# Optimization experiments

Measured on AMD Instinct MI355X. Metric: run time of the kernel, lower is better.

The kernel has to match this reference:

```python
import jax, jax.numpy as jnp
import numpy as np

T = 64        # n_estimators
DEPTH = 8
D = 2**DEPTH - 1   # internal nodes per tree (255)
K = 2**DEPTH       # leaves per tree (256)
M = 512       # n_features
C = 8         # class_num
B = 4096      # batch


def _build_path_masks():
    # Complete binary tree in heap order. For leaf l, walk from root;
    # going LEFT corresponds to b==+1 -> multiply (1 - x_node) -> Bpos,
    # going RIGHT corresponds to b==-1 -> multiply x_node -> Bneg.
    Bpos = np.zeros((K, D), dtype=np.float32)
    Bneg = np.zeros((K, D), dtype=np.float32)
    for l in range(K):
        node = 0
        for level in range(DEPTH):
            bit = (l >> (DEPTH - 1 - level)) & 1
            if bit == 0:
                Bpos[l, node] = 1.0
            else:
                Bneg[l, node] = 1.0
            node = 2 * node + 1 + bit
    return Bpos, Bneg


def setup_inputs() -> dict:
    rng = np.random.default_rng(0)
    key = jax.random.key(0)
    x = jax.random.normal(key, (B, M), dtype=jnp.float32)
    # fcn1: each internal node splits on one feature -> one-hot weight row,
    # bias = -threshold (change_parameters1).
    feat = rng.integers(0, M, size=(T, D))
    W1 = np.zeros((T, D, M), dtype=np.float32)
    W1[np.arange(T)[:, None], np.arange(D)[None, :], feat] = 1.0
    b1 = (-rng.standard_normal((T, D))).astype(np.float32)  # -threshold
    # Path masks shared across trees (complete trees), tiled per tree.
    Bpos1, Bneg1 = _build_path_masks()
    Bpos = np.broadcast_to(Bpos1, (T, K, D)).copy()
    Bneg = np.broadcast_to(Bneg1, (T, K, D)).copy()
    # fcn2 weight = c^T with zero bias (change_parameters2): leaf values [T, K, C]
    Cw = rng.random((T, K, C)).astype(np.float32)
    return {
        "input": x,
        "W1": jnp.asarray(W1),
        "b1": jnp.asarray(b1),
        "Bpos": jnp.asarray(Bpos),
        "Bneg": jnp.asarray(Bneg),
        "Cw": jnp.asarray(Cw),
    }


def reference(input, W1, b1, Bpos, Bneg, Cw):
    # z: [B, T, D] = 10 * (fcn1 per tree)
    z = 10.0 * (jnp.einsum("bm,tdm->btd", input, W1) + b1)
    # x = sigmoid(z); leaf-path product:
    #   x_c[b,t,k] = prod_d x^Bneg[t,k,d] * (1-x)^Bpos[t,k,d]
    # computed exactly in log-space (all factors in (0,1)):
    log_x = jax.nn.log_sigmoid(z)       # log sigmoid(z)
    log_1mx = jax.nn.log_sigmoid(-z)    # log (1 - sigmoid(z))
    log_xc = (jnp.einsum("btd,tkd->btk", log_x, Bneg)
              + jnp.einsum("btd,tkd->btk", log_1mx, Bpos))
    x_c = jnp.exp(log_xc)               # [B, T, K]
    # fcn2 (zero bias) then forest average over trees
    out = jnp.einsum("btk,tkc->bc", x_c, Cw) / T
    return out
```

## Files before the change

### kernel.cpp

```cpp
#include <hip/hip_runtime.h>
#include <hip/hip_bf16.h>

#define TT 64
#define DD 255
#define KK 256
#define MM 512
#define CC 8
#define BB 4096
#define RB 16
#define TPB 16
#define ST 18

typedef _Float16 h8 __attribute__((ext_vector_type(8)));
typedef _Float16 h2v __attribute__((ext_vector_type(2)));
typedef float f4 __attribute__((ext_vector_type(4)));

__device__ __forceinline__ h2v pkrtz(float a, float b) {
    return __builtin_bit_cast(h2v, __builtin_amdgcn_cvt_pkrtz(a, b));
}

__device__ __forceinline__ float wave_sum(float v) {
    v += __shfl_down(v, 32, 64);
    v += __shfl_down(v, 16, 64);
    v += __shfl_down(v, 8, 64);
    v += __shfl_down(v, 4, 64);
    v += __shfl_down(v, 2, 64);
    v += __shfl_down(v, 1, 64);
    return v;
}

__global__ void feat_kernel(const float* __restrict__ W1, int* __restrict__ feat) {
    const int row = blockIdx.x * 4 + (threadIdx.x >> 6);
    const int lane = threadIdx.x & 63;
    const float4* r = reinterpret_cast<const float4*>(W1 + (size_t)row * MM);
    float4 a = r[lane];
    float4 b = r[lane + 64];
    float ba = (float)(4 * lane);
    float bb = (float)(4 * (lane + 64));
    float acc = 0.0f;
    acc = fmaf(a.x, ba,        acc);
    acc = fmaf(a.y, ba + 1.0f, acc);
    acc = fmaf(a.z, ba + 2.0f, acc);
    acc = fmaf(a.w, ba + 3.0f, acc);
    acc = fmaf(b.x, bb,        acc);
    acc = fmaf(b.y, bb + 1.0f, acc);
    acc = fmaf(b.z, bb + 2.0f, acc);
    acc = fmaf(b.w, bb + 3.0f, acc);
    acc = wave_sum(acc);
    if (lane == 0) feat[row] = (int)(acc + 0.5f);
}

__global__ void cwt_kernel(const float* __restrict__ Cw, _Float16* __restrict__ cwT) {
    int idx = blockIdx.x * 256 + threadIdx.x;
    int t = idx >> 8, k = idx & 255;
    int c = k >> 5, sl = (k >> 3) & 3, j = k & 7;
    const float4* p = reinterpret_cast<const float4*>(Cw + (size_t)idx * CC);
    float4 p0 = p[0], p1 = p[1];
    _Float16* base = cwT + ((((t * 8 + c) * 8) * 4 + sl) * 8 + j);
    base[0 * 32] = (_Float16)p0.x;
    base[1 * 32] = (_Float16)p0.y;
    base[2 * 32] = (_Float16)p0.z;
    base[3 * 32] = (_Float16)p0.w;
    base[4 * 32] = (_Float16)p1.x;
    base[5 * 32] = (_Float16)p1.y;
    base[6 * 32] = (_Float16)p1.z;
    base[7 * 32] = (_Float16)p1.w;
}

__device__ __forceinline__ float sigm_from(float xv, float c1) {
    float earg = fmaf(-14.426950408889634f, xv, c1);
    float e = exp2f(earg);
    return __builtin_amdgcn_rcpf(1.0f + e);
}

__global__ __launch_bounds__(256, 2) void forest_kernel(
        const float* __restrict__ x, const float* __restrict__ b1,
        const _Float16* __restrict__ cwT, const int* __restrict__ feat,
        float* __restrict__ out) {
    __shared__ __align__(16) _Float16 xsi[(MM / 2) * 34];
    __shared__ _Float16 s8[4][256 * ST];

    const int tid = threadIdx.x;
    const int w = tid >> 6;
    const int lane = tid & 63;
    const int b0 = blockIdx.x * RB;
    const int t0 = blockIdx.y * TPB;
    const int m = lane & 15;
    const int slot = lane >> 4;

    for (int idx = tid; idx < MM * RB; idx += 256) {
        int mm = idx & (MM - 1);
        int r = idx >> 9;
        xsi[17 * mm - (mm & 1) + r] = (_Float16)x[(size_t)(b0 + r) * MM + mm];
    }
    __syncthreads();

    _Float16* s8w = s8[w];

    const int b3 = slot >> 1, b4 = slot & 1;
    const float sg3 = (float)(2 * b3 - 1), off3 = (float)(1 - b3);
    const float sg4 = (float)(2 * b4 - 1), off4 = (float)(1 - b4);

    f4 acc = {0.f, 0.f, 0.f, 0.f};

    for (int tt = 0; tt < 4; ++tt) {
        const int t = t0 + w * 4 + tt;
        asm volatile("" ::: "memory");

        #pragma unroll
        for (int kq = 0; kq < 4; ++kq) {
            int d = kq * 64 + lane;
            if (d < DD) {
                int f = feat[t * DD + d];
                float c1 = -14.426950408889634f * b1[t * DD + d];
                const uint32_t* xp = reinterpret_cast<const uint32_t*>(xsi) + ((17 * f) >> 1);
                uint32_t* sp = reinterpret_cast<uint32_t*>(s8w + d * ST);
                #pragma unroll
                for (int i2 = 0; i2 < 8; ++i2) {
                    h2v u = __builtin_bit_cast(h2v, xp[i2]);
                    float sa = sigm_from((float)u.x, c1);
                    float sb = sigm_from((float)u.y, c1);
                    sp[i2] = __builtin_bit_cast(uint32_t, pkrtz(sa, sb));
                }
            }
        }

        h8 bfr[8] = {};
        if (m < CC) {
            const h8* cp = reinterpret_cast<const h8*>(cwT) +
                           (((t * 8 + 0) * 8 + m) * 4 + slot);
            #pragma unroll
            for (int c = 0; c < 8; ++c) bfr[c] = cp[c * 32];
        }
        asm volatile("s_waitcnt lgkmcnt(0)" ::: "memory");

        float s0 = (float)s8w[0 * ST + m];
        float s1 = (float)s8w[1 * ST + m];
        float s2 = (float)s8w[2 * ST + m];
        float s3 = (float)s8w[3 * ST + m];
        float s4 = (float)s8w[4 * ST + m];
        float s5p = (float)s8w[5 * ST + m];
        float s6 = (float)s8w[6 * ST + m];
        float P10 = 1.0f - s0, P11 = s0;
        float P200 = P10 * (1.0f - s1), P201 = P10 * s1;
        float P210 = P11 * (1.0f - s2), P211 = P11 * s2;
        float P3a[8];
        P3a[0] = P200 * (1.0f - s3); P3a[1] = P200 * s3;
        P3a[2] = P201 * (1.0f - s4); P3a[3] = P201 * s4;
        P3a[4] = P210 * (1.0f - s5p); P3a[5] = P210 * s5p;
        P3a[6] = P211 * (1.0f - s6); P3a[7] = P211 * s6;

        #pragma unroll
        for (int c = 0; c < 8; ++c) {
            const int n3 = 7 + c;
            float sc3 = (float)s8w[n3 * ST + m];
            float f3 = fmaf(sg3, sc3, off3);
            int n4 = 2 * n3 + 1 + b3;
            float sc4 = (float)s8w[n4 * ST + m];
            float f4v = fmaf(sg4, sc4, off4);
            float P5 = P3a[c] * f3 * f4v;
            int n5 = 2 * n4 + 1 + b4;
            float s5 = (float)s8w[n5 * ST + m];
            float v1 = P5 * s5, v0 = P5 - v1;
            int q0 = 2 * n5 + 1;
            float sq0 = (float)s8w[q0 * ST + m];
            float sq1 = (float)s8w[(q0 + 1) * ST + m];
            float w01 = v0 * sq0, w00 = v0 - w01;
            float w11 = v1 * sq1, w10 = v1 - w11;
            int r0 = 2 * q0 + 1;
            float sr0 = (float)s8w[(r0 + 0) * ST + m];
            float sr1 = (float)s8w[(r0 + 1) * ST + m];
            float sr2 = (float)s8w[(r0 + 2) * ST + m];
            float sr3 = (float)s8w[(r0 + 3) * ST + m];
            float l1 = w00 * sr0, l0 = w00 - l1;
            float l3 = w01 * sr1, l2 = w01 - l3;
            float l5 = w10 * sr2, l4 = w10 - l5;
            float l7 = w11 * sr3, l6 = w11 - l7;
            union { h8 v; h2v p[4]; } U;
            U.p[0] = pkrtz(l0, l1);
            U.p[1] = pkrtz(l2, l3);
            U.p[2] = pkrtz(l4, l5);
            U.p[3] = pkrtz(l6, l7);
            acc = __builtin_amdgcn_mfma_f32_16x16x32_f16(U.v, bfr[c], acc, 0, 0, 0);
        }
    }

    __syncthreads();
    f4* red = reinterpret_cast<f4*>(xsi);
    red[w * 64 + lane] = acc;
    __syncthreads();
    if (tid < 64) {
        f4 sum = red[0 * 64 + tid];
        sum += red[1 * 64 + tid];
        sum += red[2 * 64 + tid];
        sum += red[3 * 64 + tid];
        int n = tid & 15, sl = tid >> 4;
        if (n < CC) {
            #pragma unroll
            for (int reg = 0; reg < 4; ++reg) {
                int row = sl * 4 + reg;
                atomicAdd(&out[(size_t)(b0 + row) * CC + n], sum[reg] * (1.0f / 64.0f));
            }
        }
    }
}

extern "C" void kernel_launch(void* const* d_in, const int* in_sizes, int n_in,
                              void* d_out, int out_size, void* d_ws, size_t ws_size,
                              hipStream_t stream) {
    const float* x  = (const float*)d_in[0];
    const float* W1 = (const float*)d_in[1];
    const float* b1 = (const float*)d_in[2];
    const float* Cw = (const float*)d_in[5];
    float* out = (float*)d_out;

    _Float16* cwT = (_Float16*)d_ws;
    int* feat = (int*)((char*)d_ws + (size_t)TT * KK * CC * sizeof(_Float16));

    (void)hipMemsetAsync(out, 0, (size_t)BB * CC * sizeof(float), stream);
    feat_kernel<<<(TT * DD) / 4, 256, 0, stream>>>(W1, feat);
    cwt_kernel<<<(TT * KK) / 256, 256, 0, stream>>>(Cw, cwT);
    forest_kernel<<<dim3(BB / RB, TT / TPB), 256, 0, stream>>>(x, b1, cwT, feat, out);
}
```

Before: 147.4 us.

## Prefetch next tree's split metadata and vectorize shared x loads

Changes the shared-memory layout of the staged input rows from an odd-stride skewed layout to a plain 16-element stride. Each feature's 16 half values can then be read with two 128-bit LDS loads instead of eight 32-bit loads. The per-tree feature index and bias loads are software-pipelined one tree ahead in registers so global latency overlaps with the sigmoid and MFMA work, and the tree loop is fully unrolled. The cost is higher register pressure, and the 16-half stride may cause LDS bank conflicts when lanes read random feature rows.

```diff
diff --git a/kernel.cpp b/kernel.cpp
--- a/kernel.cpp
+++ b/kernel.cpp
@@ -10,10 +10,12 @@
 #define RB 16
 #define TPB 16
 #define ST 18
+#define XS 16
 
 typedef _Float16 h8 __attribute__((ext_vector_type(8)));
 typedef _Float16 h2v __attribute__((ext_vector_type(2)));
 typedef float f4 __attribute__((ext_vector_type(4)));
+typedef uint32_t u32a __attribute__((may_alias));
 
 __device__ __forceinline__ h2v pkrtz(float a, float b) {
     return __builtin_bit_cast(h2v, __builtin_amdgcn_cvt_pkrtz(a, b));
@@ -77,7 +79,7 @@
         const float* __restrict__ x, const float* __restrict__ b1,
         const _Float16* __restrict__ cwT, const int* __restrict__ feat,
         float* __restrict__ out) {
-    __shared__ __align__(16) _Float16 xsi[(MM / 2) * 34];
+    __shared__ __align__(16) _Float16 xsi[MM * XS];
     __shared__ _Float16 s8[4][256 * ST];
 
     const int tid = threadIdx.x;
@@ -91,7 +93,7 @@
     for (int idx = tid; idx < MM * RB; idx += 256) {
         int mm = idx & (MM - 1);
         int r = idx >> 9;
-        xsi[17 * mm - (mm & 1) + r] = (_Float16)x[(size_t)(b0 + r) * MM + mm];
+        xsi[mm * XS + r] = (_Float16)x[(size_t)(b0 + r) * MM + mm];
     }
     __syncthreads();
 
@@ -103,27 +105,22 @@
 
     f4 acc = {0.f, 0.f, 0.f, 0.f};
 
+    auto ldmeta = [&](int t, int kq, int& f, float& c1) {
+        int d = kq * 64 + lane;
+        int idx = t * DD + (d < DD ? d : 0);
+        f = feat[idx];
+        c1 = -14.426950408889634f * b1[idx];
+    };
+
+    int fcur[4]; float ccur[4];
+    #pragma unroll
+    for (int kq = 0; kq < 4; ++kq) ldmeta(t0 + w * 4, kq, fcur[kq], ccur[kq]);
+
+    #pragma unroll
     for (int tt = 0; tt < 4; ++tt) {
         const int t = t0 + w * 4 + tt;
+
         asm volatile("" ::: "memory");
-
-        #pragma unroll
-        for (int kq = 0; kq < 4; ++kq) {
-            int d = kq * 64 + lane;
-            if (d < DD) {
-                int f = feat[t * DD + d];
-                float c1 = -14.426950408889634f * b1[t * DD + d];
-                const uint32_t* xp = reinterpret_cast<const uint32_t*>(xsi) + ((17 * f) >> 1);
-                uint32_t* sp = reinterpret_cast<uint32_t*>(s8w + d * ST);
-                #pragma unroll
-                for (int i2 = 0; i2 < 8; ++i2) {
-                    h2v u = __builtin_bit_cast(h2v, xp[i2]);
-                    float sa = sigm_from((float)u.x, c1);
-                    float sb = sigm_from((float)u.y, c1);
-                    sp[i2] = __builtin_bit_cast(uint32_t, pkrtz(sa, sb));
-                }
-            }
-        }
 
         h8 bfr[8] = {};
         if (m < CC) {
@@ -131,6 +128,37 @@
                            (((t * 8 + 0) * 8 + m) * 4 + slot);
             #pragma unroll
             for (int c = 0; c < 8; ++c) bfr[c] = cp[c * 32];
+        }
+
+        int fnxt[4]; float cnxt[4];
+        #pragma unroll
+        for (int kq = 0; kq < 4; ++kq) { fnxt[kq] = fcur[kq]; cnxt[kq] = ccur[kq]; }
+        if (tt < 3) {
+            #pragma unroll
+            for (int kq = 0; kq < 4; ++kq) ldmeta(t + 1, kq, fnxt[kq], cnxt[kq]);
+        }
+
+        #pragma unroll
+        for (int kq = 0; kq < 4; ++kq) {
+            int d = kq * 64 + lane;
+            if (d < DD) {
+                const float4* xp = reinterpret_cast<const float4*>(xsi + fcur[kq] * XS);
+                float4 A = xp[0], Bv = xp[1];
+                float c1 = ccur[kq];
+                u32a* sp = reinterpret_cast<u32a*>(s8w + d * ST);
+                uint32_t raw[8] = {
+                    __builtin_bit_cast(uint32_t, A.x), __builtin_bit_cast(uint32_t, A.y),
+                    __builtin_bit_cast(uint32_t, A.z), __builtin_bit_cast(uint32_t, A.w),
+                    __builtin_bit_cast(uint32_t, Bv.x), __builtin_bit_cast(uint32_t, Bv.y),
+                    __builtin_bit_cast(uint32_t, Bv.z), __builtin_bit_cast(uint32_t, Bv.w)};
+                #pragma unroll
+                for (int i2 = 0; i2 < 8; ++i2) {
+                    h2v u = __builtin_bit_cast(h2v, raw[i2]);
+                    float sa = sigm_from((float)u.x, c1);
+                    float sb = sigm_from((float)u.y, c1);
+                    sp[i2] = __builtin_bit_cast(uint32_t, pkrtz(sa, sb));
+                }
+            }
         }
         asm volatile("s_waitcnt lgkmcnt(0)" ::: "memory");
 
@@ -183,6 +211,9 @@
             U.p[3] = pkrtz(l6, l7);
             acc = __builtin_amdgcn_mfma_f32_16x16x32_f16(U.v, bfr[c], acc, 0, 0, 0);
         }
+
+        #pragma unroll
+        for (int kq = 0; kq < 4; ++kq) { fcur[kq] = fnxt[kq]; ccur[kq] = cnxt[kq]; }
     }
 
     __syncthreads();
```

After: 141.7 us. 1.04x faster.

## Compute node sigmoids on demand per lane instead of staging all nodes in LDS

Applied to the files above, without the earlier changes.

Drops the per-wave LDS stage that computed sigmoids for all 255 nodes times 16 rows. Each lane now computes only the node sigmoids on its own leaf path, directly from the transposed x tile. A new meta kernel precomputes per-lane node feature indices and scaled biases in vectorized layouts, so the hot loop reads int4/float4 metadata from global memory. This removes the LDS write/read round trip and the stage's shared memory, but adds redundant sigmoid evaluations across lanes that share upper nodes, plus many small global metadata loads.

```diff
diff --git a/kernel.cpp b/kernel.cpp
--- a/kernel.cpp
+++ b/kernel.cpp
@@ -9,7 +9,7 @@
 #define BB 4096
 #define RB 16
 #define TPB 16
-#define ST 18
+#define XS 16
 
 typedef _Float16 h8 __attribute__((ext_vector_type(8)));
 typedef _Float16 h2v __attribute__((ext_vector_type(2)));
@@ -67,6 +67,32 @@
     base[7 * 32] = (_Float16)p1.w;
 }
 
+__global__ void meta_kernel(const int* __restrict__ feat, const float* __restrict__ b1,
+                            int4* __restrict__ m46f, float4* __restrict__ m46c,
+                            int4* __restrict__ m7f, float4* __restrict__ m7c,
+                            int* __restrict__ mPf, float* __restrict__ mPc) {
+    int idx = blockIdx.x * 256 + threadIdx.x;
+    if (idx >= TT * 32) return;
+    int t = idx >> 5, rem = idx & 31;
+    int c = rem >> 2, sl = rem & 3;
+    int b3 = sl >> 1, b4 = sl & 1;
+    int base = t * DD;
+    const float K1 = -14.426950408889634f;
+    int n4 = base + 15 + 2 * c + b3;
+    int n5 = base + 31 + 4 * c + 2 * b3 + b4;
+    int q0 = base + 63 + 8 * c + 4 * b3 + 2 * b4;
+    m46f[idx] = make_int4(feat[n4], feat[n5], feat[q0], feat[q0 + 1]);
+    m46c[idx] = make_float4(K1 * b1[n4], K1 * b1[n5], K1 * b1[q0], K1 * b1[q0 + 1]);
+    int r0 = base + 127 + 16 * c + 4 * sl;
+    m7f[idx] = make_int4(feat[r0], feat[r0 + 1], feat[r0 + 2], feat[r0 + 3]);
+    m7c[idx] = make_float4(K1 * b1[r0], K1 * b1[r0 + 1], K1 * b1[r0 + 2], K1 * b1[r0 + 3]);
+    if (rem < 16) {
+        int nd = rem;
+        mPf[t * 16 + nd] = (nd < 15) ? feat[base + nd] : 0;
+        mPc[t * 16 + nd] = (nd < 15) ? K1 * b1[base + nd] : 0.0f;
+    }
+}
+
 __device__ __forceinline__ float sigm_from(float xv, float c1) {
     float earg = fmaf(-14.426950408889634f, xv, c1);
     float e = exp2f(earg);
@@ -74,11 +100,12 @@
 }
 
 __global__ __launch_bounds__(256, 2) void forest_kernel(
-        const float* __restrict__ x, const float* __restrict__ b1,
-        const _Float16* __restrict__ cwT, const int* __restrict__ feat,
+        const float* __restrict__ x, const _Float16* __restrict__ cwT,
+        const int4* __restrict__ m46f, const float4* __restrict__ m46c,
+        const int4* __restrict__ m7f, const float4* __restrict__ m7c,
+        const int* __restrict__ mPf, const float* __restrict__ mPc,
         float* __restrict__ out) {
-    __shared__ __align__(16) _Float16 xsi[(MM / 2) * 34];
-    __shared__ _Float16 s8[4][256 * ST];
+    __shared__ __align__(16) _Float16 xsi[MM * XS];
 
     const int tid = threadIdx.x;
     const int w = tid >> 6;
@@ -91,11 +118,9 @@
     for (int idx = tid; idx < MM * RB; idx += 256) {
         int mm = idx & (MM - 1);
         int r = idx >> 9;
-        xsi[17 * mm - (mm & 1) + r] = (_Float16)x[(size_t)(b0 + r) * MM + mm];
+        xsi[mm * XS + r] = (_Float16)x[(size_t)(b0 + r) * MM + mm];
     }
     __syncthreads();
-
-    _Float16* s8w = s8[w];
 
     const int b3 = slot >> 1, b4 = slot & 1;
     const float sg3 = (float)(2 * b3 - 1), off3 = (float)(1 - b3);
@@ -103,27 +128,13 @@
 
     f4 acc = {0.f, 0.f, 0.f, 0.f};
 
+    auto sigx = [&](int f, float c1) {
+        return sigm_from((float)xsi[f * XS + m], c1);
+    };
+
+    #pragma unroll
     for (int tt = 0; tt < 4; ++tt) {
         const int t = t0 + w * 4 + tt;
-        asm volatile("" ::: "memory");
-
-        #pragma unroll
-        for (int kq = 0; kq < 4; ++kq) {
-            int d = kq * 64 + lane;
-            if (d < DD) {
-                int f = feat[t * DD + d];
-                float c1 = -14.426950408889634f * b1[t * DD + d];
-                const uint32_t* xp = reinterpret_cast<const uint32_t*>(xsi) + ((17 * f) >> 1);
-                uint32_t* sp = reinterpret_cast<uint32_t*>(s8w + d * ST);
-                #pragma unroll
-                for (int i2 = 0; i2 < 8; ++i2) {
-                    h2v u = __builtin_bit_cast(h2v, xp[i2]);
-                    float sa = sigm_from((float)u.x, c1);
-                    float sb = sigm_from((float)u.y, c1);
-                    sp[i2] = __builtin_bit_cast(uint32_t, pkrtz(sa, sb));
-                }
-            }
-        }
 
         h8 bfr[8] = {};
         if (m < CC) {
@@ -132,46 +143,56 @@
             #pragma unroll
             for (int c = 0; c < 8; ++c) bfr[c] = cp[c * 32];
         }
-        asm volatile("s_waitcnt lgkmcnt(0)" ::: "memory");
-
-        float s0 = (float)s8w[0 * ST + m];
-        float s1 = (float)s8w[1 * ST + m];
-        float s2 = (float)s8w[2 * ST + m];
-        float s3 = (float)s8w[3 * ST + m];
-        float s4 = (float)s8w[4 * ST + m];
-        float s5p = (float)s8w[5 * ST + m];
-        float s6 = (float)s8w[6 * ST + m];
-        float P10 = 1.0f - s0, P11 = s0;
-        float P200 = P10 * (1.0f - s1), P201 = P10 * s1;
-        float P210 = P11 * (1.0f - s2), P211 = P11 * s2;
+
+        const int4* pf = reinterpret_cast<const int4*>(mPf + t * 16);
+        const float4* pc = reinterpret_cast<const float4*>(mPc + t * 16);
+        int4 F0 = pf[0], F1 = pf[1], F2 = pf[2], F3 = pf[3];
+        float4 C0 = pc[0], C1 = pc[1], C2 = pc[2], C3 = pc[3];
+        float sp0 = sigx(F0.x, C0.x), sp1 = sigx(F0.y, C0.y);
+        float sp2 = sigx(F0.z, C0.z), sp3 = sigx(F0.w, C0.w);
+        float sp4 = sigx(F1.x, C1.x), sp5 = sigx(F1.y, C1.y);
+        float sp6 = sigx(F1.z, C1.z);
+        float sD3[8];
+        sD3[0] = sigx(F1.w, C1.w);
+        sD3[1] = sigx(F2.x, C2.x);
+        sD3[2] = sigx(F2.y, C2.y);
+        sD3[3] = sigx(F2.z, C2.z);
+        sD3[4] = sigx(F2.w, C2.w);
+        sD3[5] = sigx(F3.x, C3.x);
+        sD3[6] = sigx(F3.y, C3.y);
+        sD3[7] = sigx(F3.z, C3.z);
+
+        float P10 = 1.0f - sp0, P11 = sp0;
+        float P200 = P10 * (1.0f - sp1), P201 = P10 * sp1;
+        float P210 = P11 * (1.0f - sp2), P211 = P11 * sp2;
         float P3a[8];
-        P3a[0] = P200 * (1.0f - s3); P3a[1] = P200 * s3;
-        P3a[2] = P201 * (1.0f - s4); P3a[3] = P201 * s4;
-        P3a[4] = P210 * (1.0f - s5p); P3a[5] = P210 * s5p;
-        P3a[6] = P211 * (1.0f - s6); P3a[7] = P211 * s6;
-
+        P3a[0] = P200 * (1.0f - sp3); P3a[1] = P200 * sp3;
+        P3a[2] = P201 * (1.0f - sp4); P3a[3] = P201 * sp4;
+        P3a[4] = P210 * (1.0f - sp5); P3a[5] = P210 * sp5;
+        P3a[6] = P211 * (1.0f - sp6); P3a[7] = P211 * sp6;
+
+        const int mbase = t * 32 + slot;
         #pragma unroll
         for (int c = 0; c < 8; ++c) {
-            const int n3 = 7 + c;
-            float sc3 = (float)s8w[n3 * ST + m];
-            float f3 = fmaf(sg3, sc3, off3);
-            int n4 = 2 * n3 + 1 + b3;
-            float sc4 = (float)s8w[n4 * ST + m];
-            float f4v = fmaf(sg4, sc4, off4);
+            int mi = mbase + c * 4;
+            int4 f46 = m46f[mi];
+            float4 c46 = m46c[mi];
+            int4 f7 = m7f[mi];
+            float4 c7 = m7c[mi];
+            float f3 = fmaf(sg3, sD3[c], off3);
+            float s4 = sigx(f46.x, c46.x);
+            float f4v = fmaf(sg4, s4, off4);
             float P5 = P3a[c] * f3 * f4v;
-            int n5 = 2 * n4 + 1 + b4;
-            float s5 = (float)s8w[n5 * ST + m];
+            float s5 = sigx(f46.y, c46.y);
             float v1 = P5 * s5, v0 = P5 - v1;
-            int q0 = 2 * n5 + 1;
-            float sq0 = (float)s8w[q0 * ST + m];
-            float sq1 = (float)s8w[(q0 + 1) * ST + m];
+            float sq0 = sigx(f46.z, c46.z);
+            float sq1 = sigx(f46.w, c46.w);
             float w01 = v0 * sq0, w00 = v0 - w01;
             float w11 = v1 * sq1, w10 = v1 - w11;
-            int r0 = 2 * q0 + 1;
-            float sr0 = (float)s8w[(r0 + 0) * ST + m];
-            float sr1 = (float)s8w[(r0 + 1) * ST + m];
-            float sr2 = (float)s8w[(r0 + 2) * ST + m];
-            float sr3 = (float)s8w[(r0 + 3) * ST + m];
+            float sr0 = sigx(f7.x, c7.x);
+            float sr1 = sigx(f7.y, c7.y);
+            float sr2 = sigx(f7.z, c7.z);
+            float sr3 = sigx(f7.w, c7.w);
             float l1 = w00 * sr0, l0 = w00 - l1;
             float l3 = w01 * sr1, l2 = w01 - l3;
             float l5 = w10 * sr2, l4 = w10 - l5;
@@ -214,11 +235,21 @@
     const float* Cw = (const float*)d_in[5];
     float* out = (float*)d_out;
 
-    _Float16* cwT = (_Float16*)d_ws;
-    int* feat = (int*)((char*)d_ws + (size_t)TT * KK * CC * sizeof(_Float16));
+    char* wsb = (char*)d_ws;
+    _Float16* cwT = (_Float16*)wsb;
+    int* feat   = (int*)(wsb + 262144);
+    int4* m46f  = (int4*)(wsb + 327680);
+    float4* m46c = (float4*)(wsb + 360448);
+    int4* m7f   = (int4*)(wsb + 393216);
+    float4* m7c = (float4*)(wsb + 425984);
+    int* mPf    = (int*)(wsb + 458752);
+    float* mPc  = (float*)(wsb + 462848);
 
     (void)hipMemsetAsync(out, 0, (size_t)BB * CC * sizeof(float), stream);
     feat_kernel<<<(TT * DD) / 4, 256, 0, stream>>>(W1, feat);
     cwt_kernel<<<(TT * KK) / 256, 256, 0, stream>>>(Cw, cwT);
-    forest_kernel<<<dim3(BB / RB, TT / TPB), 256, 0, stream>>>(x, b1, cwT, feat, out);
-}
+    meta_kernel<<<(TT * 32 + 255) / 256, 256, 0, stream>>>(feat, b1, m46f, m46c,
+                                                           m7f, m7c, mPf, mPc);
+    forest_kernel<<<dim3(BB / RB, TT / TPB), 256, 0, stream>>>(
+        x, cwT, m46f, m46c, m7f, m7c, mPf, mPc, out);
+}
```

Result: no change. 148.3 us (+0.6%).
